# Optimization experiments

Measured on AMD Instinct MI355X. Metric: run time of the kernel, lower is better.

The kernel has to match this reference:

```python
import jax, jax.numpy as jnp
import numpy as np

DIM = 1024
N_HEADS = 16
HEAD_DIM = DIM // N_HEADS
LN_EPS = 1e-5


def layer_norm(x, gamma, beta):
    mu = jnp.mean(x, axis=-1, keepdims=True)
    var = jnp.var(x, axis=-1, keepdims=True)
    return (x - mu) * jax.lax.rsqrt(var + LN_EPS) * gamma + beta


def setup_inputs() -> dict:
    key = jax.random.key(0)
    ks = jax.random.split(key, 12)
    B, Nq, Nc, D = 2, 2048, 2048, DIM
    s = 1.0 / np.sqrt(D)
    return {
        "query": jax.random.normal(ks[0], (B, Nq, D), jnp.float32),
        "context": jax.random.normal(ks[1], (B, Nc, D), jnp.float32),
        "Wq": jax.random.normal(ks[2], (D, D), jnp.float32) * s,
        "bq": jnp.zeros((D,), jnp.float32),
        "Wk": jax.random.normal(ks[3], (D, D), jnp.float32) * s,
        "bk": jnp.zeros((D,), jnp.float32),
        "Wv": jax.random.normal(ks[4], (D, D), jnp.float32) * s,
        "bv": jnp.zeros((D,), jnp.float32),
        "Wo": jax.random.normal(ks[5], (D, D), jnp.float32) * s,
        "bo": jnp.zeros((D,), jnp.float32),
        "gq": jnp.ones((D,), jnp.float32),
        "betaq": jnp.zeros((D,), jnp.float32),
        "gkv": jnp.ones((D,), jnp.float32),
        "betakv": jnp.zeros((D,), jnp.float32),
    }


def reference(query, context, Wq, bq, Wk, bk, Wv, bv, Wo, bo, gq, betaq, gkv, betakv):
    B, Nq, D = query.shape
    Nc = context.shape[1]
    residual = query
    q = layer_norm(query, gq, betaq)
    c = layer_norm(context, gkv, betakv)
    # projections; (B,N,D) -> (B,H,N,hd)
    Q = (q @ Wq + bq).reshape(B, Nq, N_HEADS, HEAD_DIM).transpose(0, 2, 1, 3)
    K = (c @ Wk + bk).reshape(B, Nc, N_HEADS, HEAD_DIM).transpose(0, 2, 1, 3)
    V = (c @ Wv + bv).reshape(B, Nc, N_HEADS, HEAD_DIM).transpose(0, 2, 1, 3)
    scores = jnp.einsum("bhqd,bhkd->bhqk", Q, K) / np.sqrt(HEAD_DIM).astype(np.float32)
    attn = jax.nn.softmax(scores, axis=-1)
    out = jnp.einsum("bhqk,bhkd->bhqd", attn, V)
    out = out.transpose(0, 2, 1, 3).reshape(B, Nq, D)
    return residual + out @ Wo + bo
```

## Files before the change

### kernel.cpp

```cpp
#include <hip/hip_runtime.h>
#include <hip/hip_bf16.h>

typedef unsigned short u16;
typedef unsigned long long u64;
typedef __bf16 bf16x8 __attribute__((ext_vector_type(8)));
typedef float f32x4 __attribute__((ext_vector_type(4)));
typedef float f32x16 __attribute__((ext_vector_type(16)));
typedef unsigned u32x4 __attribute__((ext_vector_type(4)));

#define DIM 1024
#define NH 16
#define HD 64
#define QSCALE 0.180336880972788f

__device__ __forceinline__ u16 f2bf(float f) {
  union { float f; unsigned u; } v; v.f = f;
  unsigned r = v.u + 0x7fffu + ((v.u >> 16) & 1u);
  return (u16)(r >> 16);
}

__device__ __forceinline__ unsigned pk2(float a, float b) {
  union { __hip_bfloat162 h; unsigned u; } cv;
  cv.h = __float22bfloat162_rn(make_float2(a, b));
  return cv.u;
}

__device__ __forceinline__ float bf2f(unsigned s) {
  union { unsigned u; float f; } v; v.u = s << 16; return v.f;
}

__device__ __forceinline__ float fexp2(float x) {
#if __has_builtin(__builtin_amdgcn_exp2f)
  return __builtin_amdgcn_exp2f(x);
#else
  return exp2f(x);
#endif
}

__device__ __forceinline__ void gld16(const u16* gp, u16* lp) {
  __builtin_amdgcn_global_load_lds(
      (const __attribute__((address_space(1))) unsigned int*)(const void*)gp,
      (__attribute__((address_space(3))) unsigned int*)(void*)lp, 16, 0, 0);
}

__device__ __forceinline__ void pl32swap(unsigned& a, unsigned& b) {
  asm volatile("v_permlane32_swap_b32 %0, %1" : "+v"(a), "+v"(b));
}

__device__ __forceinline__ void drain_vm_barrier() {
  asm volatile("s_waitcnt vmcnt(0)" ::: "memory");
  __builtin_amdgcn_s_barrier();
}

__global__ __launch_bounds__(256) void prep_kernel(
    const float* __restrict__ q, const float* __restrict__ c,
    const float* __restrict__ gq, const float* __restrict__ bq,
    const float* __restrict__ gkv, const float* __restrict__ bkv,
    u16* __restrict__ qn, u16* __restrict__ cn,
    const float* W0, const float* W1, const float* W2, const float* W3,
    u16* O0, u16* O1, u16* O2, u16* O3) {
  __shared__ float red[2][4];
  __shared__ float t[32][33];
  int bid = blockIdx.x, tid = threadIdx.x;
  if (bid < 8192) {
    const float* x  = bid < 4096 ? q : c;
    const float* g  = bid < 4096 ? gq : gkv;
    const float* be = bid < 4096 ? bq : bkv;
    u16* out = bid < 4096 ? qn : cn;
    int row = bid & 4095;
    float4 v = ((const float4*)(x + (size_t)row * DIM))[tid];
    float s1 = v.x + v.y + v.z + v.w;
    float s2 = v.x * v.x + v.y * v.y + v.z * v.z + v.w * v.w;
#pragma unroll
    for (int o = 32; o >= 1; o >>= 1) { s1 += __shfl_xor(s1, o, 64); s2 += __shfl_xor(s2, o, 64); }
    int wv = tid >> 6;
    if ((tid & 63) == 0) { red[0][wv] = s1; red[1][wv] = s2; }
    __syncthreads();
    s1 = red[0][0] + red[0][1] + red[0][2] + red[0][3];
    s2 = red[1][0] + red[1][1] + red[1][2] + red[1][3];
    float mu = s1 * (1.f / DIM);
    float var = s2 * (1.f / DIM) - mu * mu;
    float rs = rsqrtf(var + 1e-5f);
    float4 gv = ((const float4*)g)[tid];
    float4 bv = ((const float4*)be)[tid];
    uint2 o2;
    o2.x = pk2((v.x - mu) * rs * gv.x + bv.x, (v.y - mu) * rs * gv.y + bv.y);
    o2.y = pk2((v.z - mu) * rs * gv.z + bv.z, (v.w - mu) * rs * gv.w + bv.w);
    ((uint2*)(out + (size_t)row * DIM))[tid] = o2;
  } else {
    int wid = bid - 8192;
    int z = wid >> 10;
    const float* W = z == 0 ? W0 : z == 1 ? W1 : z == 2 ? W2 : W3;
    u16* O        = z == 0 ? O0 : z == 1 ? O1 : z == 2 ? O2 : O3;
    int xy = wid & 1023;
    int bx = (xy & 31) * 32, by = (xy >> 5) * 32;
    int tx = tid & 31, ty = tid >> 5;
#pragma unroll
    for (int i = 0; i < 4; ++i) t[ty + i * 8][tx] = W[(size_t)(by + ty + i * 8) * DIM + bx + tx];
    __syncthreads();
#pragma unroll
    for (int i = 0; i < 4; ++i) O[(size_t)(bx + ty + i * 8) * DIM + by + tx] = f2bf(t[tx][ty + i * 8]);
  }
}

#define QKV_BUF 16384
__global__ __launch_bounds__(256) void gemm_qkv(
    const u16* __restrict__ qn, const u16* __restrict__ cn,
    const u16* __restrict__ Wqt, const u16* __restrict__ Wkt, const u16* __restrict__ Wvt,
    const float* __restrict__ bq, const float* __restrict__ bk, const float* __restrict__ bv,
    u16* __restrict__ Qb, u16* __restrict__ Kb, u16* __restrict__ Vtb) {
  __shared__ __align__(16) u16 sm[2 * QKV_BUF];
  int tid = threadIdx.x, wave = tid >> 6, lane = tid & 63;
  int lr = lane & 15, quad = lane >> 4;
  int m0 = blockIdx.x * 128, n0 = blockIdx.y * 64;
  int wm = (wave >> 1) * 64, wn = (wave & 1) * 32;

  if (blockIdx.z == 0) {
    auto stage = [&](int buf, int kt) {
      u16* As  = sm + buf * QKV_BUF;
      u16* B0s = As + 128 * 64;
      u16* B1s = As + 192 * 64;
#pragma unroll
      for (int r = 0; r < 4; ++r) {
        int slot = tid + r * 256;
        int row = slot >> 3;
        int c = (slot & 7) ^ (row & 7);
        gld16(cn + (size_t)(m0 + row) * DIM + kt + c * 8, &As[slot * 8]);
      }
#pragma unroll
      for (int r = 0; r < 2; ++r) {
        int slot = tid + r * 256;
        int row = slot >> 3;
        int c = (slot & 7) ^ (row & 7);
        gld16(Wkt + (size_t)(n0 + row) * DIM + kt + c * 8, &B0s[slot * 8]);
        gld16(Wvt + (size_t)(n0 + row) * DIM + kt + c * 8, &B1s[slot * 8]);
      }
    };

    f32x4 acck[4][2] = {}, accv[4][2] = {};
    stage(0, 0);
    drain_vm_barrier();
    int cur = 0;
    for (int kt = 0; kt < DIM; kt += 64) {
      if (kt + 64 < DIM) stage(cur ^ 1, kt + 64);
      const u16* As  = sm + cur * QKV_BUF;
      const u16* B0s = As + 128 * 64;
      const u16* B1s = As + 192 * 64;
#pragma unroll
      for (int kc = 0; kc < 2; ++kc) {
        int pc = ((kc * 4 + quad) ^ (lr & 7)) * 8;
        bf16x8 af[4], b0f[2], b1f[2];
#pragma unroll
        for (int i = 0; i < 4; ++i) af[i] = *(const bf16x8*)&As[(wm + i * 16 + lr) * 64 + pc];
#pragma unroll
        for (int j = 0; j < 2; ++j) {
          b0f[j] = *(const bf16x8*)&B0s[(wn + j * 16 + lr) * 64 + pc];
          b1f[j] = *(const bf16x8*)&B1s[(wn + j * 16 + lr) * 64 + pc];
        }
#pragma unroll
        for (int mi = 0; mi < 4; ++mi)
#pragma unroll
          for (int ni = 0; ni < 2; ++ni) {
            acck[mi][ni] = __builtin_amdgcn_mfma_f32_16x16x32_bf16(af[mi], b0f[ni], acck[mi][ni], 0, 0, 0);
            accv[mi][ni] = __builtin_amdgcn_mfma_f32_16x16x32_bf16(b1f[ni], af[mi], accv[mi][ni], 0, 0, 0);
          }
      }
      drain_vm_barrier();
      cur ^= 1;
    }
#pragma unroll
    for (int mi = 0; mi < 4; ++mi)
#pragma unroll
      for (int ni = 0; ni < 2; ++ni) {
        int col = n0 + wn + ni * 16 + lr;
        float bb_ = bk[col];
        int row0 = m0 + wm + mi * 16 + quad * 4;
#pragma unroll
        for (int r = 0; r < 4; ++r)
          Kb[(size_t)(row0 + r) * DIM + col] = f2bf(acck[mi][ni][r] + bb_);
      }
#pragma unroll
    for (int mi = 0; mi < 4; ++mi) {
      int m = m0 + wm + mi * 16 + lr;
      int bb = m >> 11, tt = m & 2047;
      u16* outb = Vtb + (((size_t)bb << 10)) * 2048 + tt;
#pragma unroll
      for (int ni = 0; ni < 2; ++ni) {
        int nbase = n0 + wn + ni * 16 + quad * 4;
#pragma unroll
        for (int r = 0; r < 4; ++r)
          outb[(size_t)(nbase + r) * 2048] = f2bf(accv[mi][ni][r] + bv[nbase + r]);
      }
    }
  } else {
    auto stage = [&](int buf, int kt) {
      u16* As  = sm + buf * QKV_BUF;
      u16* B0s = As + 128 * 64;
#pragma unroll
      for (int r = 0; r < 4; ++r) {
        int slot = tid + r * 256;
        int row = slot >> 3;
        int c = (slot & 7) ^ (row & 7);
        gld16(qn + (size_t)(m0 + row) * DIM + kt + c * 8, &As[slot * 8]);
      }
#pragma unroll
      for (int r = 0; r < 2; ++r) {
        int slot = tid + r * 256;
        int row = slot >> 3;
        int c = (slot & 7) ^ (row & 7);
        gld16(Wqt + (size_t)(n0 + row) * DIM + kt + c * 8, &B0s[slot * 8]);
      }
    };

    f32x4 acc[4][2] = {};
    stage(0, 0);
    drain_vm_barrier();
    int cur = 0;
    for (int kt = 0; kt < DIM; kt += 64) {
      if (kt + 64 < DIM) stage(cur ^ 1, kt + 64);
      const u16* As  = sm + cur * QKV_BUF;
      const u16* B0s = As + 128 * 64;
#pragma unroll
      for (int kc = 0; kc < 2; ++kc) {
        int pc = ((kc * 4 + quad) ^ (lr & 7)) * 8;
        bf16x8 af[4], b0f[2];
#pragma unroll
        for (int i = 0; i < 4; ++i) af[i] = *(const bf16x8*)&As[(wm + i * 16 + lr) * 64 + pc];
#pragma unroll
        for (int j = 0; j < 2; ++j) b0f[j] = *(const bf16x8*)&B0s[(wn + j * 16 + lr) * 64 + pc];
#pragma unroll
        for (int mi = 0; mi < 4; ++mi)
#pragma unroll
          for (int ni = 0; ni < 2; ++ni)
            acc[mi][ni] = __builtin_amdgcn_mfma_f32_16x16x32_bf16(af[mi], b0f[ni], acc[mi][ni], 0, 0, 0);
      }
      drain_vm_barrier();
      cur ^= 1;
    }
#pragma unroll
    for (int mi = 0; mi < 4; ++mi)
#pragma unroll
      for (int ni = 0; ni < 2; ++ni) {
        int col = n0 + wn + ni * 16 + lr;
        float bb_ = bq[col];
        int row0 = m0 + wm + mi * 16 + quad * 4;
#pragma unroll
        for (int r = 0; r < 4; ++r)
          Qb[(size_t)(row0 + r) * DIM + col] = f2bf((acc[mi][ni][r] + bb_) * QSCALE);
      }
  }
}

#define O_BUF 12288
__global__ __launch_bounds__(256) void gemm_o(const u16* __restrict__ A,
    const u16* __restrict__ Bt, const float* __restrict__ bias,
    float* __restrict__ out, const float* __restrict__ resid) {
  __shared__ __align__(16) u16 sm[2 * O_BUF];
  int tid = threadIdx.x, wave = tid >> 6, lane = tid & 63;
  int lr = lane & 15, quad = lane >> 4;
  int m0 = blockIdx.x * 128, n0 = blockIdx.y * 64;
  int wm = (wave >> 1) * 64, wn = (wave & 1) * 32;

  auto stage = [&](int buf, int kt) {
    u16* As = sm + buf * O_BUF;
    u16* Bs = As + 128 * 64;
#pragma unroll
    for (int r = 0; r < 4; ++r) {
      int slot = tid + r * 256;
      int row = slot >> 3;
      int c = (slot & 7) ^ (row & 7);
      gld16(A + (size_t)(m0 + row) * DIM + kt + c * 8, &As[slot * 8]);
    }
#pragma unroll
    for (int r = 0; r < 2; ++r) {
      int slot = tid + r * 256;
      int row = slot >> 3;
      int c = (slot & 7) ^ (row & 7);
      gld16(Bt + (size_t)(n0 + row) * DIM + kt + c * 8, &Bs[slot * 8]);
    }
  };

  f32x4 acc[4][2] = {};
  stage(0, 0);
  drain_vm_barrier();
  int cur = 0;
  for (int kt = 0; kt < DIM; kt += 64) {
    if (kt + 64 < DIM) stage(cur ^ 1, kt + 64);
    const u16* As = sm + cur * O_BUF;
    const u16* Bs = As + 128 * 64;
#pragma unroll
    for (int kc = 0; kc < 2; ++kc) {
      int pc = ((kc * 4 + quad) ^ (lr & 7)) * 8;
      bf16x8 af[4], bfr[2];
#pragma unroll
      for (int i = 0; i < 4; ++i) af[i] = *(const bf16x8*)&As[(wm + i * 16 + lr) * 64 + pc];
#pragma unroll
      for (int j = 0; j < 2; ++j) bfr[j] = *(const bf16x8*)&Bs[(wn + j * 16 + lr) * 64 + pc];
#pragma unroll
      for (int mi = 0; mi < 4; ++mi)
#pragma unroll
        for (int ni = 0; ni < 2; ++ni)
          acc[mi][ni] = __builtin_amdgcn_mfma_f32_16x16x32_bf16(af[mi], bfr[ni], acc[mi][ni], 0, 0, 0);
    }
    drain_vm_barrier();
    cur ^= 1;
  }
#pragma unroll
  for (int mi = 0; mi < 4; ++mi)
#pragma unroll
    for (int ni = 0; ni < 2; ++ni) {
      int col = n0 + wn + ni * 16 + lr;
      float bv = bias[col];
      int row0 = m0 + wm + mi * 16 + quad * 4;
#pragma unroll
      for (int r = 0; r < 4; ++r) {
        int row = row0 + r;
        out[(size_t)row * DIM + col] = acc[mi][ni][r] + bv + resid[(size_t)row * DIM + col];
      }
    }
}

__global__ __launch_bounds__(256, 2) void flash_kernel(const u16* __restrict__ Q,
    const u16* __restrict__ Kg, const u16* __restrict__ Vt, u16* __restrict__ AO) {
  __shared__ __align__(16) u16 lds[32768];
  int tid = threadIdx.x, wave = tid >> 6, lane = tid & 63;
  int ln = lane & 31, hi = lane >> 5;
  int bh = blockIdx.x, b = bh >> 4, h = bh & 15;
  int q0 = blockIdx.y * 128;

  const u16* kbase = Kg + (size_t)(b * 2048) * DIM + h * HD;
  const u16* vbase = Vt + (size_t)(b * 1024 + h * HD) * 2048;

  size_t qrow = (size_t)(b * 2048 + q0 + wave * 32 + ln);
  bf16x8 qf[4];
#pragma unroll
  for (int ds = 0; ds < 4; ++ds)
    qf[ds] = *(const bf16x8*)&Q[qrow * DIM + h * HD + ds * 16 + hi * 8];

  int slot0 = tid, slot1 = tid + 256;
  int r0 = slot0 >> 3, c0 = (slot0 & 7) ^ (r0 & 7);
  int r1 = slot1 >> 3, c1 = (slot1 & 7) ^ (r1 & 7);
  const u16* kp0 = kbase + (size_t)r0 * DIM + c0 * 8;
  const u16* kp1 = kbase + (size_t)r1 * DIM + c1 * 8;
  const u16* vp0 = vbase + (size_t)r0 * 2048 + c0 * 8;
  const u16* vp1 = vbase + (size_t)r1 * 2048 + c1 * 8;

#pragma unroll
  for (int t = 0; t < 2; ++t) {
    gld16(kp0, &lds[t * 4096 + slot0 * 8]);
    gld16(kp1, &lds[t * 4096 + slot1 * 8]);
    gld16(vp0, &lds[16384 + t * 4096 + slot0 * 8]);
    gld16(vp1, &lds[16384 + t * 4096 + slot1 * 8]);
    kp0 += 64 * DIM; kp1 += 64 * DIM; vp0 += 64; vp1 += 64;
  }
  drain_vm_barrier();

  float plsum = 0.f;
  f32x16 oacc[2] = {};

  for (int j = 0; j < 32; j += 2) {
    if (j + 2 < 32) {
#pragma unroll
      for (int t = 0; t < 2; ++t) {
        int bi = (j + 2 + t) & 3;
        gld16(kp0, &lds[bi * 4096 + slot0 * 8]);
        gld16(kp1, &lds[bi * 4096 + slot1 * 8]);
        gld16(vp0, &lds[16384 + bi * 4096 + slot0 * 8]);
        gld16(vp1, &lds[16384 + bi * 4096 + slot1 * 8]);
        kp0 += 64 * DIM; kp1 += 64 * DIM; vp0 += 64; vp1 += 64;
      }
    }

#pragma unroll
    for (int jj = 0; jj < 2; ++jj) {
      int bi = (j + jj) & 3;
      const u16* kcb = &lds[bi * 4096];
      const u16* vcb = &lds[16384 + bi * 4096];

      f32x16 sf[2] = {};
      __builtin_amdgcn_s_setprio(1);
#pragma unroll
      for (int kt2 = 0; kt2 < 2; ++kt2) {
        int rs = (kt2 * 32 + ln) * 64;
        int rx = (kt2 * 32 + ln) & 7;
#pragma unroll
        for (int ds = 0; ds < 4; ++ds) {
          bf16x8 kf = *(const bf16x8*)&kcb[rs + (((ds * 2 + hi) ^ rx) * 8)];
          sf[kt2] = __builtin_amdgcn_mfma_f32_32x32x16_bf16(kf, qf[ds], sf[kt2], 0, 0, 0);
        }
      }
      __builtin_amdgcn_s_setprio(0);

      bf16x8 pb[4];
#pragma unroll
      for (int kt2 = 0; kt2 < 2; ++kt2)
#pragma unroll
        for (int ks = 0; ks < 2; ++ks) {
          float e0 = fexp2(sf[kt2][ks * 8 + 0]), e1 = fexp2(sf[kt2][ks * 8 + 1]);
          float e2 = fexp2(sf[kt2][ks * 8 + 2]), e3 = fexp2(sf[kt2][ks * 8 + 3]);
          float e4 = fexp2(sf[kt2][ks * 8 + 4]), e5 = fexp2(sf[kt2][ks * 8 + 5]);
          float e6 = fexp2(sf[kt2][ks * 8 + 6]), e7 = fexp2(sf[kt2][ks * 8 + 7]);
          plsum += ((e0 + e1) + (e2 + e3)) + ((e4 + e5) + (e6 + e7));
          unsigned w0 = pk2(e0, e1), w1 = pk2(e2, e3);
          unsigned w2 = pk2(e4, e5), w3 = pk2(e6, e7);
          pl32swap(w0, w2);
          pl32swap(w1, w3);
          u32x4 t; t.x = w0; t.y = w1; t.z = w2; t.w = w3;
          pb[kt2 * 2 + ks] = __builtin_bit_cast(bf16x8, t);
        }

      __builtin_amdgcn_s_setprio(1);
#pragma unroll
      for (int dt = 0; dt < 2; ++dt) {
        int rs = (dt * 32 + ln) * 64;
        int rx = (dt * 32 + ln) & 7;
#pragma unroll
        for (int kk = 0; kk < 4; ++kk) {
          bf16x8 vf = *(const bf16x8*)&vcb[rs + (((kk * 2 + hi) ^ rx) * 8)];
          oacc[dt] = __builtin_amdgcn_mfma_f32_32x32x16_bf16(vf, pb[kk], oacc[dt], 0, 0, 0);
        }
      }
      __builtin_amdgcn_s_setprio(0);
    }
    drain_vm_barrier();
  }

  float l = plsum + __shfl_xor(plsum, 32, 64);
  float rl = 1.f / l;
#pragma unroll
  for (int dt = 0; dt < 2; ++dt)
#pragma unroll
    for (int g = 0; g < 4; ++g) {
      uint2 pk;
      pk.x = pk2(oacc[dt][g * 4 + 0] * rl, oacc[dt][g * 4 + 1] * rl);
      pk.y = pk2(oacc[dt][g * 4 + 2] * rl, oacc[dt][g * 4 + 3] * rl);
      *(uint2*)&AO[qrow * DIM + h * HD + dt * 32 + g * 8 + hi * 4] = pk;
    }
}

extern "C" void kernel_launch(void* const* d_in, const int* in_sizes, int n_in,
                              void* d_out, int out_size, void* d_ws, size_t ws_size,
                              hipStream_t stream) {
  const float* query   = (const float*)d_in[0];
  const float* context = (const float*)d_in[1];
  const float* Wq = (const float*)d_in[2];
  const float* bq = (const float*)d_in[3];
  const float* Wk = (const float*)d_in[4];
  const float* bk = (const float*)d_in[5];
  const float* Wv = (const float*)d_in[6];
  const float* bv = (const float*)d_in[7];
  const float* Wo = (const float*)d_in[8];
  const float* bo = (const float*)d_in[9];
  const float* gq    = (const float*)d_in[10];
  const float* betaq = (const float*)d_in[11];
  const float* gkv   = (const float*)d_in[12];
  const float* betakv= (const float*)d_in[13];
  (void)in_sizes; (void)n_in; (void)out_size; (void)ws_size;

  char* ws = (char*)d_ws;
  const size_t MB = (size_t)1 << 20;
  u16* qn  = (u16*)(ws + 0 * MB);
  u16* cn  = (u16*)(ws + 8 * MB);
  u16* Wqt = (u16*)(ws + 16 * MB);
  u16* Wkt = (u16*)(ws + 18 * MB);
  u16* Wvt = (u16*)(ws + 20 * MB);
  u16* Wot = (u16*)(ws + 22 * MB);
  u16* Qb  = (u16*)(ws + 24 * MB);
  u16* Kb  = (u16*)(ws + 32 * MB);
  u16* Vtb = (u16*)(ws + 40 * MB);
  u16* AOb = (u16*)(ws + 48 * MB);

  prep_kernel<<<12288, 256, 0, stream>>>(query, context, gq, betaq, gkv, betakv,
                                         qn, cn, Wq, Wk, Wv, Wo, Wqt, Wkt, Wvt, Wot);

  gemm_qkv<<<dim3(32, 16, 2), 256, 0, stream>>>(qn, cn, Wqt, Wkt, Wvt,
                                                bq, bk, bv, Qb, Kb, Vtb);

  flash_kernel<<<dim3(32, 16), 256, 0, stream>>>(Qb, Kb, Vtb, AOb);

  gemm_o<<<dim3(32, 16), 256, 0, stream>>>(AOb, Wot, bo, (float*)d_out, query);
}
```

Measured before the change: 203.0 us.

## Unify QKV GEMM into uniform 128x128 tiles with one block per projection

The QKV projection kernel drops its asymmetric split, where z=0 blocks did both K and V (128x64 tiles each) and z=1 blocks did Q alone. It now uses a uniform 128x128 tile per block with blockIdx.z picking Q, K or V, giving balanced work across 768 blocks. The V transpose epilogue is rewritten to compute V as A*W and write 4 consecutive tokens per lane as a packed uint2, replacing scattered 2-byte stores. Larger tiles double per-wave accumulators to 16 f32x4, raising register pressure and possibly lowering occupancy.

```diff
diff --git a/kernel.cpp b/kernel.cpp
--- a/kernel.cpp
+++ b/kernel.cpp
@@ -103,150 +103,89 @@
   }
 }
 
-#define QKV_BUF 16384
+#define G_BUF 16384
 __global__ __launch_bounds__(256) void gemm_qkv(
     const u16* __restrict__ qn, const u16* __restrict__ cn,
     const u16* __restrict__ Wqt, const u16* __restrict__ Wkt, const u16* __restrict__ Wvt,
     const float* __restrict__ bq, const float* __restrict__ bk, const float* __restrict__ bv,
     u16* __restrict__ Qb, u16* __restrict__ Kb, u16* __restrict__ Vtb) {
-  __shared__ __align__(16) u16 sm[2 * QKV_BUF];
+  __shared__ __align__(16) u16 sm[2 * G_BUF];
   int tid = threadIdx.x, wave = tid >> 6, lane = tid & 63;
   int lr = lane & 15, quad = lane >> 4;
-  int m0 = blockIdx.x * 128, n0 = blockIdx.y * 64;
-  int wm = (wave >> 1) * 64, wn = (wave & 1) * 32;
-
-  if (blockIdx.z == 0) {
-    auto stage = [&](int buf, int kt) {
-      u16* As  = sm + buf * QKV_BUF;
-      u16* B0s = As + 128 * 64;
-      u16* B1s = As + 192 * 64;
-#pragma unroll
-      for (int r = 0; r < 4; ++r) {
-        int slot = tid + r * 256;
-        int row = slot >> 3;
-        int c = (slot & 7) ^ (row & 7);
-        gld16(cn + (size_t)(m0 + row) * DIM + kt + c * 8, &As[slot * 8]);
-      }
-#pragma unroll
-      for (int r = 0; r < 2; ++r) {
-        int slot = tid + r * 256;
-        int row = slot >> 3;
-        int c = (slot & 7) ^ (row & 7);
-        gld16(Wkt + (size_t)(n0 + row) * DIM + kt + c * 8, &B0s[slot * 8]);
-        gld16(Wvt + (size_t)(n0 + row) * DIM + kt + c * 8, &B1s[slot * 8]);
-      }
-    };
-
-    f32x4 acck[4][2] = {}, accv[4][2] = {};
-    stage(0, 0);
+  int z = blockIdx.z;
+  const u16* A = (z == 2) ? qn : cn;
+  const u16* W = (z == 0) ? Wkt : (z == 1) ? Wvt : Wqt;
+  int m0 = blockIdx.x * 128, n0 = blockIdx.y * 128;
+  int wm = (wave >> 1) * 64, wn = (wave & 1) * 64;
+
+  auto stage = [&](int buf, int kt) {
+    u16* As = sm + buf * G_BUF;
+    u16* Bs = As + 128 * 64;
+#pragma unroll
+    for (int r = 0; r < 4; ++r) {
+      int slot = tid + r * 256;
+      int row = slot >> 3;
+      int c = (slot & 7) ^ (row & 7);
+      gld16(A + (size_t)(m0 + row) * DIM + kt + c * 8, &As[slot * 8]);
+      gld16(W + (size_t)(n0 + row) * DIM + kt + c * 8, &Bs[slot * 8]);
+    }
+  };
+
+  f32x4 acc[4][4] = {};
+  stage(0, 0);
+  drain_vm_barrier();
+  int cur = 0;
+  for (int kt = 0; kt < DIM; kt += 64) {
+    if (kt + 64 < DIM) stage(cur ^ 1, kt + 64);
+    const u16* As = sm + cur * G_BUF;
+    const u16* Bs = As + 128 * 64;
+#pragma unroll
+    for (int kc = 0; kc < 2; ++kc) {
+      int pc = ((kc * 4 + quad) ^ (lr & 7)) * 8;
+      bf16x8 af[4], bf[4];
+#pragma unroll
+      for (int i = 0; i < 4; ++i) af[i] = *(const bf16x8*)&As[(wm + i * 16 + lr) * 64 + pc];
+#pragma unroll
+      for (int j = 0; j < 4; ++j) bf[j] = *(const bf16x8*)&Bs[(wn + j * 16 + lr) * 64 + pc];
+#pragma unroll
+      for (int mi = 0; mi < 4; ++mi)
+#pragma unroll
+        for (int ni = 0; ni < 4; ++ni)
+          acc[mi][ni] = __builtin_amdgcn_mfma_f32_16x16x32_bf16(af[mi], bf[ni], acc[mi][ni], 0, 0, 0);
+    }
     drain_vm_barrier();
-    int cur = 0;
-    for (int kt = 0; kt < DIM; kt += 64) {
-      if (kt + 64 < DIM) stage(cur ^ 1, kt + 64);
-      const u16* As  = sm + cur * QKV_BUF;
-      const u16* B0s = As + 128 * 64;
-      const u16* B1s = As + 192 * 64;
-#pragma unroll
-      for (int kc = 0; kc < 2; ++kc) {
-        int pc = ((kc * 4 + quad) ^ (lr & 7)) * 8;
-        bf16x8 af[4], b0f[2], b1f[2];
-#pragma unroll
-        for (int i = 0; i < 4; ++i) af[i] = *(const bf16x8*)&As[(wm + i * 16 + lr) * 64 + pc];
-#pragma unroll
-        for (int j = 0; j < 2; ++j) {
-          b0f[j] = *(const bf16x8*)&B0s[(wn + j * 16 + lr) * 64 + pc];
-          b1f[j] = *(const bf16x8*)&B1s[(wn + j * 16 + lr) * 64 + pc];
-        }
-#pragma unroll
-        for (int mi = 0; mi < 4; ++mi)
-#pragma unroll
-          for (int ni = 0; ni < 2; ++ni) {
-            acck[mi][ni] = __builtin_amdgcn_mfma_f32_16x16x32_bf16(af[mi], b0f[ni], acck[mi][ni], 0, 0, 0);
-            accv[mi][ni] = __builtin_amdgcn_mfma_f32_16x16x32_bf16(b1f[ni], af[mi], accv[mi][ni], 0, 0, 0);
-          }
-      }
-      drain_vm_barrier();
-      cur ^= 1;
-    }
+    cur ^= 1;
+  }
+
+  if (z == 1) {
+#pragma unroll
+    for (int mi = 0; mi < 4; ++mi) {
+      int tok0 = m0 + wm + mi * 16 + quad * 4;
+      int bb = tok0 >> 11, tt = tok0 & 2047;
+#pragma unroll
+      for (int ni = 0; ni < 4; ++ni) {
+        int channel = n0 + wn + ni * 16 + lr;
+        float bb_ = bv[channel];
+        uint2 o;
+        o.x = pk2(acc[mi][ni][0] + bb_, acc[mi][ni][1] + bb_);
+        o.y = pk2(acc[mi][ni][2] + bb_, acc[mi][ni][3] + bb_);
+        *(uint2*)&Vtb[(((size_t)bb << 10) + channel) * 2048 + tt] = o;
+      }
+    }
+  } else {
+    const float* bias = (z == 0) ? bk : bq;
+    u16* out = (z == 0) ? Kb : Qb;
+    float scale = (z == 0) ? 1.f : QSCALE;
 #pragma unroll
     for (int mi = 0; mi < 4; ++mi)
 #pragma unroll
-      for (int ni = 0; ni < 2; ++ni) {
+      for (int ni = 0; ni < 4; ++ni) {
         int col = n0 + wn + ni * 16 + lr;
-        float bb_ = bk[col];
+        float bb_ = bias[col];
         int row0 = m0 + wm + mi * 16 + quad * 4;
 #pragma unroll
         for (int r = 0; r < 4; ++r)
-          Kb[(size_t)(row0 + r) * DIM + col] = f2bf(acck[mi][ni][r] + bb_);
-      }
-#pragma unroll
-    for (int mi = 0; mi < 4; ++mi) {
-      int m = m0 + wm + mi * 16 + lr;
-      int bb = m >> 11, tt = m & 2047;
-      u16* outb = Vtb + (((size_t)bb << 10)) * 2048 + tt;
-#pragma unroll
-      for (int ni = 0; ni < 2; ++ni) {
-        int nbase = n0 + wn + ni * 16 + quad * 4;
-#pragma unroll
-        for (int r = 0; r < 4; ++r)
-          outb[(size_t)(nbase + r) * 2048] = f2bf(accv[mi][ni][r] + bv[nbase + r]);
-      }
-    }
-  } else {
-    auto stage = [&](int buf, int kt) {
-      u16* As  = sm + buf * QKV_BUF;
-      u16* B0s = As + 128 * 64;
-#pragma unroll
-      for (int r = 0; r < 4; ++r) {
-        int slot = tid + r * 256;
-        int row = slot >> 3;
-        int c = (slot & 7) ^ (row & 7);
-        gld16(qn + (size_t)(m0 + row) * DIM + kt + c * 8, &As[slot * 8]);
-      }
-#pragma unroll
-      for (int r = 0; r < 2; ++r) {
-        int slot = tid + r * 256;
-        int row = slot >> 3;
-        int c = (slot & 7) ^ (row & 7);
-        gld16(Wqt + (size_t)(n0 + row) * DIM + kt + c * 8, &B0s[slot * 8]);
-      }
-    };
-
-    f32x4 acc[4][2] = {};
-    stage(0, 0);
-    drain_vm_barrier();
-    int cur = 0;
-    for (int kt = 0; kt < DIM; kt += 64) {
-      if (kt + 64 < DIM) stage(cur ^ 1, kt + 64);
-      const u16* As  = sm + cur * QKV_BUF;
-      const u16* B0s = As + 128 * 64;
-#pragma unroll
-      for (int kc = 0; kc < 2; ++kc) {
-        int pc = ((kc * 4 + quad) ^ (lr & 7)) * 8;
-        bf16x8 af[4], b0f[2];
-#pragma unroll
-        for (int i = 0; i < 4; ++i) af[i] = *(const bf16x8*)&As[(wm + i * 16 + lr) * 64 + pc];
-#pragma unroll
-        for (int j = 0; j < 2; ++j) b0f[j] = *(const bf16x8*)&B0s[(wn + j * 16 + lr) * 64 + pc];
-#pragma unroll
-        for (int mi = 0; mi < 4; ++mi)
-#pragma unroll
-          for (int ni = 0; ni < 2; ++ni)
-            acc[mi][ni] = __builtin_amdgcn_mfma_f32_16x16x32_bf16(af[mi], b0f[ni], acc[mi][ni], 0, 0, 0);
-      }
-      drain_vm_barrier();
-      cur ^= 1;
-    }
-#pragma unroll
-    for (int mi = 0; mi < 4; ++mi)
-#pragma unroll
-      for (int ni = 0; ni < 2; ++ni) {
-        int col = n0 + wn + ni * 16 + lr;
-        float bb_ = bq[col];
-        int row0 = m0 + wm + mi * 16 + quad * 4;
-#pragma unroll
-        for (int r = 0; r < 4; ++r)
-          Qb[(size_t)(row0 + r) * DIM + col] = f2bf((acc[mi][ni][r] + bb_) * QSCALE);
+          out[(size_t)(row0 + r) * DIM + col] = f2bf((acc[mi][ni][r] + bb_) * scale);
       }
   }
 }
@@ -473,8 +412,8 @@
   prep_kernel<<<12288, 256, 0, stream>>>(query, context, gq, betaq, gkv, betakv,
                                          qn, cn, Wq, Wk, Wv, Wo, Wqt, Wkt, Wvt, Wot);
 
-  gemm_qkv<<<dim3(32, 16, 2), 256, 0, stream>>>(qn, cn, Wqt, Wkt, Wvt,
-                                                bq, bk, bv, Qb, Kb, Vtb);
+  gemm_qkv<<<dim3(32, 8, 3), 256, 0, stream>>>(qn, cn, Wqt, Wkt, Wvt,
+                                               bq, bk, bv, Qb, Kb, Vtb);
 
   flash_kernel<<<dim3(32, 16), 256, 0, stream>>>(Qb, Kb, Vtb, AOb);
 
```

Result: slower. 218.2 us (+7.5%).

## Load K/V fragments directly from global into registers, dropping LDS staging

Applied to the files above, without the earlier changes.

The flash attention kernel no longer stages K and V tiles in shared memory with async global-to-LDS copies and barriers. Each wave now loads its own K and V MFMA fragments straight from global memory into registers, with K double-buffered one tile ahead and V loaded at the start of each tile. This removes LDS traffic and block-wide barriers, but the four waves of a block each fetch the same K/V data (relying on cache) and register pressure rises; the occupancy hint of 2 blocks per CU is also dropped.

```diff
diff --git a/kernel.cpp b/kernel.cpp
--- a/kernel.cpp
+++ b/kernel.cpp
@@ -320,110 +320,87 @@
     }
 }
 
-__global__ __launch_bounds__(256, 2) void flash_kernel(const u16* __restrict__ Q,
+__global__ __launch_bounds__(256) void flash_kernel(const u16* __restrict__ Q,
     const u16* __restrict__ Kg, const u16* __restrict__ Vt, u16* __restrict__ AO) {
-  __shared__ __align__(16) u16 lds[32768];
   int tid = threadIdx.x, wave = tid >> 6, lane = tid & 63;
   int ln = lane & 31, hi = lane >> 5;
   int bh = blockIdx.x, b = bh >> 4, h = bh & 15;
   int q0 = blockIdx.y * 128;
 
-  const u16* kbase = Kg + (size_t)(b * 2048) * DIM + h * HD;
-  const u16* vbase = Vt + (size_t)(b * 1024 + h * HD) * 2048;
-
   size_t qrow = (size_t)(b * 2048 + q0 + wave * 32 + ln);
   bf16x8 qf[4];
 #pragma unroll
   for (int ds = 0; ds < 4; ++ds)
     qf[ds] = *(const bf16x8*)&Q[qrow * DIM + h * HD + ds * 16 + hi * 8];
 
-  int slot0 = tid, slot1 = tid + 256;
-  int r0 = slot0 >> 3, c0 = (slot0 & 7) ^ (r0 & 7);
-  int r1 = slot1 >> 3, c1 = (slot1 & 7) ^ (r1 & 7);
-  const u16* kp0 = kbase + (size_t)r0 * DIM + c0 * 8;
-  const u16* kp1 = kbase + (size_t)r1 * DIM + c1 * 8;
-  const u16* vp0 = vbase + (size_t)r0 * 2048 + c0 * 8;
-  const u16* vp1 = vbase + (size_t)r1 * 2048 + c1 * 8;
-
-#pragma unroll
-  for (int t = 0; t < 2; ++t) {
-    gld16(kp0, &lds[t * 4096 + slot0 * 8]);
-    gld16(kp1, &lds[t * 4096 + slot1 * 8]);
-    gld16(vp0, &lds[16384 + t * 4096 + slot0 * 8]);
-    gld16(vp1, &lds[16384 + t * 4096 + slot1 * 8]);
-    kp0 += 64 * DIM; kp1 += 64 * DIM; vp0 += 64; vp1 += 64;
-  }
-  drain_vm_barrier();
+  const u16* kb = Kg + ((size_t)(b * 2048 + ln)) * DIM + h * HD + hi * 8;
+  const u16* vb = Vt + ((size_t)(b * 1024 + h * HD + ln)) * 2048 + hi * 8;
+
+#define LOADK(dst, j)                                                          \
+  _Pragma("unroll")                                                            \
+  for (int kt2 = 0; kt2 < 2; ++kt2)                                            \
+    _Pragma("unroll")                                                          \
+    for (int ds = 0; ds < 4; ++ds)                                             \
+      dst[kt2 * 4 + ds] = *(const bf16x8*)(kb + ((size_t)((j) * 64 + kt2 * 32)) * DIM + ds * 16);
+
+#define LOADV(dst, j)                                                          \
+  _Pragma("unroll")                                                            \
+  for (int dt = 0; dt < 2; ++dt)                                               \
+    _Pragma("unroll")                                                          \
+    for (int kk = 0; kk < 4; ++kk)                                             \
+      dst[dt * 4 + kk] = *(const bf16x8*)(vb + (size_t)(dt * 32) * 2048 + (j) * 64 + kk * 16);
 
   float plsum = 0.f;
   f32x16 oacc[2] = {};
+  bf16x8 kA[8], kB[8], vC[8];
+
+  LOADK(kA, 0);
+
+#define HALF(KCUR, KNXT, jj, jnxt)                                             \
+  {                                                                            \
+    LOADV(vC, jj);                                                             \
+    if ((jnxt) < 32) LOADK(KNXT, jnxt);                                        \
+    f32x16 sf[2] = {};                                                         \
+    __builtin_amdgcn_s_setprio(1);                                             \
+    _Pragma("unroll")                                                          \
+    for (int kt2 = 0; kt2 < 2; ++kt2)                                          \
+      _Pragma("unroll")                                                        \
+      for (int ds = 0; ds < 4; ++ds)                                           \
+        sf[kt2] = __builtin_amdgcn_mfma_f32_32x32x16_bf16(KCUR[kt2 * 4 + ds], qf[ds], sf[kt2], 0, 0, 0); \
+    __builtin_amdgcn_s_setprio(0);                                             \
+    bf16x8 pb[4];                                                              \
+    _Pragma("unroll")                                                          \
+    for (int kt2 = 0; kt2 < 2; ++kt2)                                          \
+      _Pragma("unroll")                                                        \
+      for (int ks = 0; ks < 2; ++ks) {                                         \
+        float e0 = fexp2(sf[kt2][ks * 8 + 0]), e1 = fexp2(sf[kt2][ks * 8 + 1]);\
+        float e2 = fexp2(sf[kt2][ks * 8 + 2]), e3 = fexp2(sf[kt2][ks * 8 + 3]);\
+        float e4 = fexp2(sf[kt2][ks * 8 + 4]), e5 = fexp2(sf[kt2][ks * 8 + 5]);\
+        float e6 = fexp2(sf[kt2][ks * 8 + 6]), e7 = fexp2(sf[kt2][ks * 8 + 7]);\
+        plsum += ((e0 + e1) + (e2 + e3)) + ((e4 + e5) + (e6 + e7));            \
+        unsigned w0 = pk2(e0, e1), w1 = pk2(e2, e3);                           \
+        unsigned w2 = pk2(e4, e5), w3 = pk2(e6, e7);                           \
+        pl32swap(w0, w2);                                                      \
+        pl32swap(w1, w3);                                                      \
+        u32x4 t; t.x = w0; t.y = w1; t.z = w2; t.w = w3;                       \
+        pb[kt2 * 2 + ks] = __builtin_bit_cast(bf16x8, t);                      \
+      }                                                                        \
+    __builtin_amdgcn_s_setprio(1);                                             \
+    _Pragma("unroll")                                                          \
+    for (int dt = 0; dt < 2; ++dt)                                             \
+      _Pragma("unroll")                                                        \
+      for (int kk = 0; kk < 4; ++kk)                                           \
+        oacc[dt] = __builtin_amdgcn_mfma_f32_32x32x16_bf16(vC[dt * 4 + kk], pb[kk], oacc[dt], 0, 0, 0); \
+    __builtin_amdgcn_s_setprio(0);                                             \
+  }
 
   for (int j = 0; j < 32; j += 2) {
-    if (j + 2 < 32) {
-#pragma unroll
-      for (int t = 0; t < 2; ++t) {
-        int bi = (j + 2 + t) & 3;
-        gld16(kp0, &lds[bi * 4096 + slot0 * 8]);
-        gld16(kp1, &lds[bi * 4096 + slot1 * 8]);
-        gld16(vp0, &lds[16384 + bi * 4096 + slot0 * 8]);
-        gld16(vp1, &lds[16384 + bi * 4096 + slot1 * 8]);
-        kp0 += 64 * DIM; kp1 += 64 * DIM; vp0 += 64; vp1 += 64;
-      }
-    }
-
-#pragma unroll
-    for (int jj = 0; jj < 2; ++jj) {
-      int bi = (j + jj) & 3;
-      const u16* kcb = &lds[bi * 4096];
-      const u16* vcb = &lds[16384 + bi * 4096];
-
-      f32x16 sf[2] = {};
-      __builtin_amdgcn_s_setprio(1);
-#pragma unroll
-      for (int kt2 = 0; kt2 < 2; ++kt2) {
-        int rs = (kt2 * 32 + ln) * 64;
-        int rx = (kt2 * 32 + ln) & 7;
-#pragma unroll
-        for (int ds = 0; ds < 4; ++ds) {
-          bf16x8 kf = *(const bf16x8*)&kcb[rs + (((ds * 2 + hi) ^ rx) * 8)];
-          sf[kt2] = __builtin_amdgcn_mfma_f32_32x32x16_bf16(kf, qf[ds], sf[kt2], 0, 0, 0);
-        }
-      }
-      __builtin_amdgcn_s_setprio(0);
-
-      bf16x8 pb[4];
-#pragma unroll
-      for (int kt2 = 0; kt2 < 2; ++kt2)
-#pragma unroll
-        for (int ks = 0; ks < 2; ++ks) {
-          float e0 = fexp2(sf[kt2][ks * 8 + 0]), e1 = fexp2(sf[kt2][ks * 8 + 1]);
-          float e2 = fexp2(sf[kt2][ks * 8 + 2]), e3 = fexp2(sf[kt2][ks * 8 + 3]);
-          float e4 = fexp2(sf[kt2][ks * 8 + 4]), e5 = fexp2(sf[kt2][ks * 8 + 5]);
-          float e6 = fexp2(sf[kt2][ks * 8 + 6]), e7 = fexp2(sf[kt2][ks * 8 + 7]);
-          plsum += ((e0 + e1) + (e2 + e3)) + ((e4 + e5) + (e6 + e7));
-          unsigned w0 = pk2(e0, e1), w1 = pk2(e2, e3);
-          unsigned w2 = pk2(e4, e5), w3 = pk2(e6, e7);
-          pl32swap(w0, w2);
-          pl32swap(w1, w3);
-          u32x4 t; t.x = w0; t.y = w1; t.z = w2; t.w = w3;
-          pb[kt2 * 2 + ks] = __builtin_bit_cast(bf16x8, t);
-        }
-
-      __builtin_amdgcn_s_setprio(1);
-#pragma unroll
-      for (int dt = 0; dt < 2; ++dt) {
-        int rs = (dt * 32 + ln) * 64;
-        int rx = (dt * 32 + ln) & 7;
-#pragma unroll
-        for (int kk = 0; kk < 4; ++kk) {
-          bf16x8 vf = *(const bf16x8*)&vcb[rs + (((kk * 2 + hi) ^ rx) * 8)];
-          oacc[dt] = __builtin_amdgcn_mfma_f32_32x32x16_bf16(vf, pb[kk], oacc[dt], 0, 0, 0);
-        }
-      }
-      __builtin_amdgcn_s_setprio(0);
-    }
-    drain_vm_barrier();
+    HALF(kA, kB, j, j + 1);
+    HALF(kB, kA, j + 1, j + 2);
   }
+#undef HALF
+#undef LOADK
+#undef LOADV
 
   float l = plsum + __shfl_xor(plsum, 32, 64);
   float rl = 1.f / l;
```

New measurement: 275.4 us. 35.7% more time.
